# Performance work log

Measured on AMD Instinct MI355X. Metric: run time of the kernel, lower is better.

Reference implementation:

```python
import jax, jax.numpy as jnp
import numpy as np

N_WIRES = 10
N_BLOCKS = 4
DIM = 2 ** N_WIRES


def _tables(n):
    # Basis-state bit tables. Wire 0 is the most-significant bit (torchquantum convention).
    s = np.arange(2 ** n)
    bits = (s[None, :] >> (n - 1 - np.arange(n))[:, None]) & 1  # [n, 2^n]
    zval = (1 - 2 * bits).astype(np.float32)  # PauliZ eigenvalue per wire per basis state
    # Composition of the circular CNOT ring (0,1),(1,2),...,(n-2,n-1),(n-1,0)
    # as a single basis permutation: state'[s] = state[P[s]].
    pairs = [(i, i + 1) for i in range(n - 1)] + [(n - 1, 0)]
    P = s.copy()
    for c, t in pairs:
        bit = (s >> (n - 1 - c)) & 1
        g = s ^ (bit << (n - 1 - t))  # CNOT maps new[s] = old[g(s)]
        P = P[g]
    return zval, P


_ZVAL_NP, _PERM_NP = _tables(N_WIRES)


def setup_inputs() -> dict:
    key = jax.random.key(0)
    k1, k2 = jax.random.split(key)
    x = jax.random.normal(k1, (2048, N_WIRES), jnp.float32)
    params = jax.random.normal(k2, (N_BLOCKS, 6, N_WIRES), jnp.float32)
    return {"x": x, "params": params}


def _rz_all(state, theta, zval):
    # RZ(theta_w) on every wire fused into one diagonal phase over the full statevector.
    # RZ = diag(e^{-i t/2}, e^{+i t/2}); exponent sign = -zval (bit0 -> -1).
    phase = jnp.exp((-0.5j) * (theta @ zval).astype(jnp.complex64))  # [2^n]
    return state * phase[None, :]


def _ry_all(state, theta, bsz):
    # RY(theta_w) on each wire w: 2x2 rotation applied along that wire's axis.
    for w in range(N_WIRES):
        left = 2 ** w
        right = DIM // (2 * left)
        s4 = state.reshape(bsz, left, 2, right)
        c = jnp.cos(theta[w] * 0.5)
        s_ = jnp.sin(theta[w] * 0.5)
        U = jnp.stack([jnp.stack([c, -s_]), jnp.stack([s_, c])]).astype(jnp.complex64)
        s4 = jnp.einsum('bixk,jx->bijk', s4, U)
        state = s4.reshape(bsz, DIM)
    return state


def reference(x, params):
    zval = jnp.asarray(_ZVAL_NP)
    perm = jnp.asarray(_PERM_NP)
    bsz = x.shape[0]
    state = jnp.zeros((bsz, DIM), jnp.complex64).at[:, 0].set(1.0)  # |0...0>
    for k in range(N_BLOCKS):
        p = params[k]
        # NOTE: the original module's "rx" layers are constructed with tq.RZ,
        # so each block is RZ, RY, RZ, CNOT-ring, RZ, RY, RZ, CNOT-ring.
        state = _rz_all(state, p[0], zval)
        state = _ry_all(state, p[1], bsz)
        state = _rz_all(state, p[2], zval)
        state = state[:, perm]
        state = _rz_all(state, p[3], zval)
        state = _ry_all(state, p[4], bsz)
        state = _rz_all(state, p[5], zval)
        state = state[:, perm]
        if k != N_BLOCKS - 1:
            # data re-uploading encoder: RZ(x[:, w]) on wire w, batch-dependent diagonal
            enc = jnp.exp((-0.5j) * (x @ zval).astype(jnp.complex64))  # [B, 2^n]
            state = state * enc
    probs = state.real ** 2 + state.imag ** 2  # [B, 2^n]
    out = probs @ zval.T  # MeasureAll PauliZ -> [B, n_wires]
    return out[None]  # [1, B, n_wires]
```

## Files before the change

kernel.cpp:

```cpp
#include <hip/hip_runtime.h>

#define NW 10

template<int CTRL>
__device__ __forceinline__ float fdpp(float v) {
    return __int_as_float(__builtin_amdgcn_mov_dpp(__float_as_int(v), CTRL, 0xF, 0xF, true));
}
template<int PAT>
__device__ __forceinline__ float fswz(float v) {
    return __int_as_float(__builtin_amdgcn_ds_swizzle(__float_as_int(v), PAT));
}

__device__ __forceinline__ int sC(int W, int lane, int r) { return (W << 8) | (lane << 2) | r; }
__device__ __forceinline__ int sL1(int W, int lane, int r) {
    return ((r & 1) << 8) | (((r >> 1) & 1) << 9)
         | ((lane & 1) << 4) | (((lane >> 1) & 1) << 6) | (((lane >> 2) & 1) << 2)
         | (((lane >> 3) & 1) << 7) | (((lane >> 4) & 1) << 3) | (((lane >> 5) & 1) << 5)
         | ((W & 1) << 0) | (((W >> 1) & 1) << 1);
}
__device__ __forceinline__ int phi(int e) {
    return e ^ ((e & 0x10) >> 1) ^ ((e & 0x20) >> 4);
}

__global__ void precompute_kernel(const float* __restrict__ params, float2* __restrict__ tab) {
    const int d = blockIdx.x;
    const int j = threadIdx.x;
    if (d < 14) {
        int k, row; bool L1;
        if (d < 3)       { k = d + 1;  row = 0; L1 = false; }
        else if (d < 7)  { k = d - 3;  row = 2; L1 = true;  }
        else if (d < 11) { k = d - 7;  row = 3; L1 = false; }
        else             { k = d - 11; row = 5; L1 = true;  }
        const float* th = params + (k * 6 + row) * NW;
        const int W = j >> 8, lane = j & 63, r = (j >> 6) & 3;
        const int s = L1 ? sL1(W, lane, r) : sC(W, lane, r);
        float ang = 0.f;
#pragma unroll
        for (int w = 0; w < NW; ++w)
            ang += th[w] * (((s >> (9 - w)) & 1) ? 0.5f : -0.5f);
        float sn, cs;
        __sincosf(ang, &sn, &cs);
        tab[d * 1024 + j] = make_float2(cs, sn);
    } else if (j < 80) {
        const int ry = j / NW, w = j % NW;
        const int k = ry >> 1, i = ry & 1;
        const float* th = params + (k * 6 + (i ? 4 : 1)) * NW;
        float sn, cs;
        __sincosf(0.5f * th[w], &sn, &cs);
        tab[14 * 1024 + j] = make_float2(cs, sn);
    }
}

__global__ __launch_bounds__(256, 4) void qsim_kernel(const float* __restrict__ x,
                                                      const float2* __restrict__ tab,
                                                      float* __restrict__ out) {
    __shared__ float2 buf[2][1024];
    __shared__ float sred[4][NW];

    const int t     = threadIdx.x;
    const int W     = t >> 6;
    const int lane  = t & 63;
    const int b     = blockIdx.x;
    const int ebase = lane | (W << 8);
    const float2* ry_tab = tab + 14 * 1024;

    float re[4], im[4];
#pragma unroll
    for (int r = 0; r < 4; ++r) { re[r] = 0.f; im[r] = 0.f; }
    if (t == 0) re[0] = 1.f;

    const int wbase = phi(ebase);

    const int l0 = lane & 1, l1 = (lane >> 1) & 1, l2 = (lane >> 2) & 1,
              l3 = (lane >> 3) & 1, l4 = (lane >> 4) & 1, l5 = (lane >> 5) & 1;
    const int W0 = W & 1, W1 = (W >> 1) & 1;
    const int riA0 = l2 | (l4 << 1) | (l0 << 2) | (l5 << 3) | (l1 << 4) | (l3 << 5) | (W << 6);
    const int rgA  = phi(riA0);
    const int g0 = (l2 ^ l3) | ((l4 ^ l5) << 1) | ((l0 ^ l1) << 2) | ((l5 ^ W0) << 3)
                 | ((l1 ^ l2) << 4) | ((l3 ^ l4) << 5)
                 | ((W0 ^ W1) << 6) | (W1 << 7) | (l0 << 9);
    const int gP = phi(g0);

    const float* xb = x + b * NW;
    float xr[4], xi[4];
    {
        float xv[NW];
#pragma unroll
        for (int w = 0; w < NW; ++w) xv[w] = xb[w];
        float A = 0.f;
#pragma unroll
        for (int w = 0; w < NW; ++w) A += xv[w];
        float hi = -0.5f * A;
        if (W & 2) hi += xv[0];
        if (W & 1) hi += xv[1];
#pragma unroll
        for (int j = 0; j < 6; ++j)
            hi += ((lane >> j) & 1) ? xv[7 - j] : 0.f;
        float lo[4];
        lo[0] = 0.f;   lo[1] = xv[9];
        lo[2] = xv[8]; lo[3] = xv[8] + xv[9];
#pragma unroll
        for (int r = 0; r < 4; ++r)
            __sincosf(hi + lo[r], &xi[r], &xr[r]);
    }

    int bs = 0;

    auto tdiag = [&](int d) {
        const float2* tb = tab + (d << 10) + ebase;
#pragma unroll
        for (int r = 0; r < 4; ++r) {
            const float2 p = tb[r << 6];
            const float a = re[r], bb = im[r];
            re[r] = a * p.x - bb * p.y;
            im[r] = a * p.y + bb * p.x;
        }
    };
    auto txdiag = [&](int d) {
        const float2* tb = tab + (d << 10) + ebase;
#pragma unroll
        for (int r = 0; r < 4; ++r) {
            const float2 p = tb[r << 6];
            const float cx = p.x * xr[r] - p.y * xi[r];
            const float sx = p.x * xi[r] + p.y * xr[r];
            const float a = re[r], bb = im[r];
            re[r] = a * cx - bb * sx;
            im[r] = a * sx + bb * cx;
        }
    };

    auto bfly_local = [&](float2 cw, int m) {
#pragma unroll
        for (int r = 0; r < 4; ++r) {
            if (!(r & m)) {
                const int r2 = r | m;
                float a = re[r], bb = re[r2];
                re[r]  = cw.x * a - cw.y * bb;
                re[r2] = cw.y * a + cw.x * bb;
                float ai = im[r], bi = im[r2];
                im[r]  = cw.x * ai - cw.y * bi;
                im[r2] = cw.y * ai + cw.x * bi;
            }
        }
    };

    auto ry = [&](int ridx) {
        const float2* rt = ry_tab + ridx * NW;
        bfly_local(rt[9], 1);
        bfly_local(rt[8], 2);
        {   const float2 cw = rt[7]; const float ss = (lane & 1) ? cw.y : -cw.y;
#pragma unroll
            for (int r = 0; r < 4; ++r) {
                float pre = fdpp<0xB1>(re[r]), pim = fdpp<0xB1>(im[r]);
                re[r] = cw.x * re[r] + ss * pre;
                im[r] = cw.x * im[r] + ss * pim;
            }
        }
        {   const float2 cw = rt[6]; const float ss = (lane & 2) ? cw.y : -cw.y;
#pragma unroll
            for (int r = 0; r < 4; ++r) {
                float pre = fdpp<0x4E>(re[r]), pim = fdpp<0x4E>(im[r]);
                re[r] = cw.x * re[r] + ss * pre;
                im[r] = cw.x * im[r] + ss * pim;
            }
        }
        {   const float2 cw = rt[4]; const float ss = (lane & 8) ? cw.y : -cw.y;
#pragma unroll
            for (int r = 0; r < 4; ++r) {
                float pre = fdpp<0x128>(re[r]), pim = fdpp<0x128>(im[r]);
                re[r] = cw.x * re[r] + ss * pre;
                im[r] = cw.x * im[r] + ss * pim;
            }
        }
        {
            float2* B = buf[bs]; bs ^= 1;
#pragma unroll
            for (int r = 0; r < 4; ++r)
                B[wbase + (r << 6)] = make_float2(re[r], im[r]);
            __syncthreads();
#pragma unroll
            for (int r = 0; r < 4; ++r) {
                const float2 p = B[rgA + (r << 8)];
                re[r] = p.x;
                im[r] = p.y;
            }
        }
        bfly_local(rt[1], 1);
        bfly_local(rt[0], 2);
        {   const float2 cw = rt[5]; const float ss = (lane & 1) ? cw.y : -cw.y;
#pragma unroll
            for (int r = 0; r < 4; ++r) {
                float pre = fdpp<0xB1>(re[r]), pim = fdpp<0xB1>(im[r]);
                re[r] = cw.x * re[r] + ss * pre;
                im[r] = cw.x * im[r] + ss * pim;
            }
        }
        {   const float2 cw = rt[3]; const float ss = (lane & 2) ? cw.y : -cw.y;
#pragma unroll
            for (int r = 0; r < 4; ++r) {
                float pre = fdpp<0x4E>(re[r]), pim = fdpp<0x4E>(im[r]);
                re[r] = cw.x * re[r] + ss * pre;
                im[r] = cw.x * im[r] + ss * pim;
            }
        }
        {   const float2 cw = rt[2]; const float ss = (lane & 8) ? cw.y : -cw.y;
#pragma unroll
            for (int r = 0; r < 4; ++r) {
                float pre = fdpp<0x128>(re[r]), pim = fdpp<0x128>(im[r]);
                re[r] = cw.x * re[r] + ss * pre;
                im[r] = cw.x * im[r] + ss * pim;
            }
        }
    };

    auto perm = [&]() {
        float2* B = buf[bs]; bs ^= 1;
#pragma unroll
        for (int r = 0; r < 4; ++r)
            B[wbase + (r << 6)] = make_float2(re[r], im[r]);
        __syncthreads();
        constexpr int xc[4] = {0, 0x1C0, 0x300, 0x2C0};
#pragma unroll
        for (int r = 0; r < 4; ++r) {
            const float2 p = B[gP ^ xc[r]];
            re[r] = p.x;
            im[r] = p.y;
        }
    };

#pragma unroll 1
    for (int k = 0; k < 4; ++k) {
        if (k > 0) txdiag(k - 1);
        ry(2 * k);
        tdiag(3 + k);
        perm();
        tdiag(7 + k);
        ry(2 * k + 1);
        if (k < 3) tdiag(11 + k);
        perm();
    }

    float pr[4];
#pragma unroll
    for (int r = 0; r < 4; ++r) pr[r] = re[r] * re[r] + im[r] * im[r];
    float S = 0.f;
#pragma unroll
    for (int r = 0; r < 4; ++r) S += pr[r];

    float acc[NW];
    acc[0] = (W & 2) ? -S : S;
    acc[1] = (W & 1) ? -S : S;
#pragma unroll
    for (int w = 2; w <= 7; ++w) {
        const int j = 7 - w;
        acc[w] = ((lane >> j) & 1) ? -S : S;
    }
    {
        float t8 = 0.f, t9 = 0.f;
#pragma unroll
        for (int r = 0; r < 4; ++r) {
            t8 += (r & 2) ? -pr[r] : pr[r];
            t9 += (r & 1) ? -pr[r] : pr[r];
        }
        acc[8] = t8; acc[9] = t9;
    }
#pragma unroll
    for (int w = 0; w < NW; ++w) {
        float a = acc[w];
        a += fdpp<0xB1>(a);
        a += fdpp<0x4E>(a);
        a += fswz<0x101F>(a);
        a += fdpp<0x128>(a);
        a += fswz<0x401F>(a);
        a += __shfl_xor(a, 32, 64);
        acc[w] = a;
    }
    if (lane == 0) {
#pragma unroll
        for (int w = 0; w < NW; ++w) sred[W][w] = acc[w];
    }
    __syncthreads();
    if (t < NW) out[b * NW + t] = sred[0][t] + sred[1][t] + sred[2][t] + sred[3][t];
}

extern "C" void kernel_launch(void* const* d_in, const int* in_sizes, int n_in,
                              void* d_out, int out_size, void* d_ws, size_t ws_size,
                              hipStream_t stream) {
    const float* x      = (const float*)d_in[0];
    const float* params = (const float*)d_in[1];
    float* out          = (float*)d_out;
    float2* tab         = (float2*)d_ws;
    (void)in_sizes; (void)n_in; (void)out_size; (void)ws_size;
    precompute_kernel<<<15, 1024, 0, stream>>>(params, tab);
    qsim_kernel<<<2048, 256, 0, stream>>>(x, tab, out);
}
```

Baseline: 87.58 us.

## Vectorize complex state as float2 packed math and prefetch diagonal tables

Stores the statevector amplitudes as 2-wide float vectors so complex multiplies and butterflies can map to packed FP32 instructions, and widens the diagonal phase table to float4 (cs, sn, -sn, cs) so each complex multiply is two vector FMAs. Diagonal table loads are issued one stage early (before the RY/permutation work) so global-load latency overlaps with compute and LDS exchanges. In exchange the table doubles in size, and holding prefetched values in registers raises register pressure under the 4-blocks-per-SIMD launch bound.

```diff
diff --git a/kernel.cpp b/kernel.cpp
--- a/kernel.cpp
+++ b/kernel.cpp
@@ -1,6 +1,9 @@
 #include <hip/hip_runtime.h>
 
 #define NW 10
+
+typedef float v2f __attribute__((ext_vector_type(2)));
+typedef float v4f __attribute__((ext_vector_type(4)));
 
 template<int CTRL>
 __device__ __forceinline__ float fdpp(float v) {
@@ -22,7 +25,7 @@
     return e ^ ((e & 0x10) >> 1) ^ ((e & 0x20) >> 4);
 }
 
-__global__ void precompute_kernel(const float* __restrict__ params, float2* __restrict__ tab) {
+__global__ void precompute_kernel(const float* __restrict__ params, float4* __restrict__ tab4) {
     const int d = blockIdx.x;
     const int j = threadIdx.x;
     if (d < 14) {
@@ -40,21 +43,22 @@
             ang += th[w] * (((s >> (9 - w)) & 1) ? 0.5f : -0.5f);
         float sn, cs;
         __sincosf(ang, &sn, &cs);
-        tab[d * 1024 + j] = make_float2(cs, sn);
+        tab4[d * 1024 + j] = make_float4(cs, sn, -sn, cs);
     } else if (j < 80) {
         const int ry = j / NW, w = j % NW;
         const int k = ry >> 1, i = ry & 1;
         const float* th = params + (k * 6 + (i ? 4 : 1)) * NW;
         float sn, cs;
         __sincosf(0.5f * th[w], &sn, &cs);
-        tab[14 * 1024 + j] = make_float2(cs, sn);
+        float2* ryt = (float2*)(tab4 + 14 * 1024);
+        ryt[j] = make_float2(cs, sn);
     }
 }
 
 __global__ __launch_bounds__(256, 4) void qsim_kernel(const float* __restrict__ x,
-                                                      const float2* __restrict__ tab,
+                                                      const v4f* __restrict__ tab4,
                                                       float* __restrict__ out) {
-    __shared__ float2 buf[2][1024];
+    __shared__ v2f buf[2][1024];
     __shared__ float sred[4][NW];
 
     const int t     = threadIdx.x;
@@ -62,15 +66,14 @@
     const int lane  = t & 63;
     const int b     = blockIdx.x;
     const int ebase = lane | (W << 8);
-    const float2* ry_tab = tab + 14 * 1024;
-
-    float re[4], im[4];
-#pragma unroll
-    for (int r = 0; r < 4; ++r) { re[r] = 0.f; im[r] = 0.f; }
-    if (t == 0) re[0] = 1.f;
+    const float2* ry_tab = (const float2*)(tab4 + 14 * 1024);
+
+    v2f st[4];
+#pragma unroll
+    for (int r = 0; r < 4; ++r) st[r] = (v2f){0.f, 0.f};
+    if (t == 0) st[0].x = 1.f;
 
     const int wbase = phi(ebase);
-
     const int l0 = lane & 1, l1 = (lane >> 1) & 1, l2 = (lane >> 2) & 1,
               l3 = (lane >> 3) & 1, l4 = (lane >> 4) & 1, l5 = (lane >> 5) & 1;
     const int W0 = W & 1, W1 = (W >> 1) & 1;
@@ -82,7 +85,7 @@
     const int gP = phi(g0);
 
     const float* xb = x + b * NW;
-    float xr[4], xi[4];
+    v2f xp[4];
     {
         float xv[NW];
 #pragma unroll
@@ -100,32 +103,32 @@
         lo[0] = 0.f;   lo[1] = xv[9];
         lo[2] = xv[8]; lo[3] = xv[8] + xv[9];
 #pragma unroll
+        for (int r = 0; r < 4; ++r) {
+            float sn, cs;
+            __sincosf(hi + lo[r], &sn, &cs);
+            xp[r] = (v2f){cs, sn};
+        }
+    }
+
+    int bs = 0;
+    v4f tq[4];
+
+    auto pre = [&](int d) {
+        const v4f* tb = tab4 + (d << 10) + ebase;
+#pragma unroll
+        for (int r = 0; r < 4; ++r) tq[r] = tb[r << 6];
+    };
+    auto apply_t = [&]() {
+#pragma unroll
         for (int r = 0; r < 4; ++r)
-            __sincosf(hi + lo[r], &xi[r], &xr[r]);
-    }
-
-    int bs = 0;
-
-    auto tdiag = [&](int d) {
-        const float2* tb = tab + (d << 10) + ebase;
-#pragma unroll
-        for (int r = 0; r < 4; ++r) {
-            const float2 p = tb[r << 6];
-            const float a = re[r], bb = im[r];
-            re[r] = a * p.x - bb * p.y;
-            im[r] = a * p.y + bb * p.x;
-        }
-    };
-    auto txdiag = [&](int d) {
-        const float2* tb = tab + (d << 10) + ebase;
-#pragma unroll
-        for (int r = 0; r < 4; ++r) {
-            const float2 p = tb[r << 6];
-            const float cx = p.x * xr[r] - p.y * xi[r];
-            const float sx = p.x * xi[r] + p.y * xr[r];
-            const float a = re[r], bb = im[r];
-            re[r] = a * cx - bb * sx;
-            im[r] = a * sx + bb * cx;
+            st[r] = st[r].x * tq[r].xy + st[r].y * tq[r].zw;
+    };
+    auto apply_tx = [&]() {
+#pragma unroll
+        for (int r = 0; r < 4; ++r) {
+            const v2f c = xp[r].x * tq[r].xy + xp[r].y * tq[r].zw;
+            const v2f cq = (v2f){-c.y, c.x};
+            st[r] = st[r].x * c + st[r].y * cq;
         }
     };
 
@@ -134,12 +137,9 @@
         for (int r = 0; r < 4; ++r) {
             if (!(r & m)) {
                 const int r2 = r | m;
-                float a = re[r], bb = re[r2];
-                re[r]  = cw.x * a - cw.y * bb;
-                re[r2] = cw.y * a + cw.x * bb;
-                float ai = im[r], bi = im[r2];
-                im[r]  = cw.x * ai - cw.y * bi;
-                im[r2] = cw.y * ai + cw.x * bi;
+                const v2f a = st[r];
+                st[r]  = cw.x * a - cw.y * st[r2];
+                st[r2] = cw.y * a + cw.x * st[r2];
             }
         }
     };
@@ -151,98 +151,89 @@
         {   const float2 cw = rt[7]; const float ss = (lane & 1) ? cw.y : -cw.y;
 #pragma unroll
             for (int r = 0; r < 4; ++r) {
-                float pre = fdpp<0xB1>(re[r]), pim = fdpp<0xB1>(im[r]);
-                re[r] = cw.x * re[r] + ss * pre;
-                im[r] = cw.x * im[r] + ss * pim;
+                v2f p; p.x = fdpp<0xB1>(st[r].x); p.y = fdpp<0xB1>(st[r].y);
+                st[r] = cw.x * st[r] + ss * p;
             }
         }
         {   const float2 cw = rt[6]; const float ss = (lane & 2) ? cw.y : -cw.y;
 #pragma unroll
             for (int r = 0; r < 4; ++r) {
-                float pre = fdpp<0x4E>(re[r]), pim = fdpp<0x4E>(im[r]);
-                re[r] = cw.x * re[r] + ss * pre;
-                im[r] = cw.x * im[r] + ss * pim;
+                v2f p; p.x = fdpp<0x4E>(st[r].x); p.y = fdpp<0x4E>(st[r].y);
+                st[r] = cw.x * st[r] + ss * p;
             }
         }
         {   const float2 cw = rt[4]; const float ss = (lane & 8) ? cw.y : -cw.y;
 #pragma unroll
             for (int r = 0; r < 4; ++r) {
-                float pre = fdpp<0x128>(re[r]), pim = fdpp<0x128>(im[r]);
-                re[r] = cw.x * re[r] + ss * pre;
-                im[r] = cw.x * im[r] + ss * pim;
+                v2f p; p.x = fdpp<0x128>(st[r].x); p.y = fdpp<0x128>(st[r].y);
+                st[r] = cw.x * st[r] + ss * p;
             }
         }
         {
-            float2* B = buf[bs]; bs ^= 1;
+            v2f* B = buf[bs]; bs ^= 1;
 #pragma unroll
             for (int r = 0; r < 4; ++r)
-                B[wbase + (r << 6)] = make_float2(re[r], im[r]);
+                B[wbase + (r << 6)] = st[r];
             __syncthreads();
 #pragma unroll
-            for (int r = 0; r < 4; ++r) {
-                const float2 p = B[rgA + (r << 8)];
-                re[r] = p.x;
-                im[r] = p.y;
-            }
+            for (int r = 0; r < 4; ++r)
+                st[r] = B[rgA + (r << 8)];
         }
         bfly_local(rt[1], 1);
         bfly_local(rt[0], 2);
         {   const float2 cw = rt[5]; const float ss = (lane & 1) ? cw.y : -cw.y;
 #pragma unroll
             for (int r = 0; r < 4; ++r) {
-                float pre = fdpp<0xB1>(re[r]), pim = fdpp<0xB1>(im[r]);
-                re[r] = cw.x * re[r] + ss * pre;
-                im[r] = cw.x * im[r] + ss * pim;
+                v2f p; p.x = fdpp<0xB1>(st[r].x); p.y = fdpp<0xB1>(st[r].y);
+                st[r] = cw.x * st[r] + ss * p;
             }
         }
         {   const float2 cw = rt[3]; const float ss = (lane & 2) ? cw.y : -cw.y;
 #pragma unroll
             for (int r = 0; r < 4; ++r) {
-                float pre = fdpp<0x4E>(re[r]), pim = fdpp<0x4E>(im[r]);
-                re[r] = cw.x * re[r] + ss * pre;
-                im[r] = cw.x * im[r] + ss * pim;
+                v2f p; p.x = fdpp<0x4E>(st[r].x); p.y = fdpp<0x4E>(st[r].y);
+                st[r] = cw.x * st[r] + ss * p;
             }
         }
         {   const float2 cw = rt[2]; const float ss = (lane & 8) ? cw.y : -cw.y;
 #pragma unroll
             for (int r = 0; r < 4; ++r) {
-                float pre = fdpp<0x128>(re[r]), pim = fdpp<0x128>(im[r]);
-                re[r] = cw.x * re[r] + ss * pre;
-                im[r] = cw.x * im[r] + ss * pim;
+                v2f p; p.x = fdpp<0x128>(st[r].x); p.y = fdpp<0x128>(st[r].y);
+                st[r] = cw.x * st[r] + ss * p;
             }
         }
     };
 
     auto perm = [&]() {
-        float2* B = buf[bs]; bs ^= 1;
+        v2f* B = buf[bs]; bs ^= 1;
 #pragma unroll
         for (int r = 0; r < 4; ++r)
-            B[wbase + (r << 6)] = make_float2(re[r], im[r]);
+            B[wbase + (r << 6)] = st[r];
         __syncthreads();
         constexpr int xc[4] = {0, 0x1C0, 0x300, 0x2C0};
 #pragma unroll
-        for (int r = 0; r < 4; ++r) {
-            const float2 p = B[gP ^ xc[r]];
-            re[r] = p.x;
-            im[r] = p.y;
-        }
+        for (int r = 0; r < 4; ++r)
+            st[r] = B[gP ^ xc[r]];
     };
 
 #pragma unroll 1
     for (int k = 0; k < 4; ++k) {
-        if (k > 0) txdiag(k - 1);
+        if (k > 0) apply_tx();
+        pre(3 + k);
         ry(2 * k);
-        tdiag(3 + k);
+        apply_t();
+        pre(7 + k);
         perm();
-        tdiag(7 + k);
+        apply_t();
+        if (k < 3) pre(11 + k);
         ry(2 * k + 1);
-        if (k < 3) tdiag(11 + k);
+        if (k < 3) { apply_t(); pre(k); }
         perm();
     }
 
     float pr[4];
 #pragma unroll
-    for (int r = 0; r < 4; ++r) pr[r] = re[r] * re[r] + im[r] * im[r];
+    for (int r = 0; r < 4; ++r) pr[r] = st[r].x * st[r].x + st[r].y * st[r].y;
     float S = 0.f;
 #pragma unroll
     for (int r = 0; r < 4; ++r) S += pr[r];
@@ -289,8 +280,8 @@
     const float* x      = (const float*)d_in[0];
     const float* params = (const float*)d_in[1];
     float* out          = (float*)d_out;
-    float2* tab         = (float2*)d_ws;
+    float4* tab4        = (float4*)d_ws;
     (void)in_sizes; (void)n_in; (void)out_size; (void)ws_size;
-    precompute_kernel<<<15, 1024, 0, stream>>>(params, tab);
-    qsim_kernel<<<2048, 256, 0, stream>>>(x, tab, out);
-}
+    precompute_kernel<<<15, 1024, 0, stream>>>(params, tab4);
+    qsim_kernel<<<2048, 256, 0, stream>>>(x, (const v4f*)tab4, out);
+}
```

After: 83.49 us. -4.7%, faster.
